# Kernel optimization log

Hardware: AMD Instinct MI355X
Metric: run time of the kernel (lower is better)

## Reference

```python
import jax, jax.numpy as jnp
import numpy as np

N = 131072
D = 512        # input_dim
H = 512        # hidden_dim
E = 10         # num_experts
INIT_STD_SCALE = 0.1


def _trunc_normal(key, shape, std):
    # approximate trunc_normal_(std=std) in [-2std, 2std]
    return jnp.clip(jax.random.normal(key, shape) * std, -2.0 * std, 2.0 * std).astype(jnp.float32)


def setup_inputs() -> dict:
    key = jax.random.key(0)
    ks = jax.random.split(key, 6)
    x = jax.random.normal(ks[0], (N, D), dtype=jnp.float32)
    # router (default nn.Linear init approximated with uniform)
    lim = 1.0 / np.sqrt(D)
    Wr = jax.random.uniform(ks[1], (E, D), minval=-lim, maxval=lim, dtype=jnp.float32)
    br = jnp.zeros((E,), dtype=jnp.float32)
    # experts: trunc_normal with std = 0.1 / sqrt(fan_in), zero bias
    W1 = _trunc_normal(ks[2], (E, D, H), INIT_STD_SCALE / np.sqrt(D))   # [E, D, H]
    b1 = jnp.zeros((E, H), dtype=jnp.float32)
    W2 = _trunc_normal(ks[3], (E, H, H), INIT_STD_SCALE / np.sqrt(H))   # [E, H, H]
    b2 = jnp.zeros((E, H), dtype=jnp.float32)
    return {"x": x, "Wr": Wr, "br": br, "W1": W1, "b1": b1, "W2": W2, "b2": b2}


def reference(x, Wr, br, W1, b1, W2, b2):
    # router in fp32 (autocast disabled in original)
    logits = x.astype(jnp.float32) @ Wr.T + br          # [N, E]
    expert_ids = jnp.argmax(logits, axis=1)              # [N]
    out = jnp.zeros((x.shape[0], W2.shape[-1]), dtype=x.dtype)
    # fixed small loop over experts; dropout is identity at inference
    for e in range(W1.shape[0]):
        h = jax.nn.relu(x @ W1[e] + b1[e])                # [N, H]
        o = h @ W2[e] + b2[e]                             # [N, H]
        out = jnp.where((expert_ids == e)[:, None], o, out)
    return out, expert_ids
```

## Files before the change

### kernel.cpp

```cpp
#include <hip/hip_runtime.h>
#include <hip/hip_bf16.h>

#define N_TOK 131072
#define DIM   512
#define HID   512
#define NEXP  10

using bf16x8 = __attribute__((ext_vector_type(8))) short;
using f32x4  = __attribute__((ext_vector_type(4))) float;

__device__ __forceinline__ short f2bf(float f) {
    union { float f; unsigned u; } v; v.f = f;
    unsigned u = v.u;
    return (short)((u + 0x7FFFu + ((u >> 16) & 1u)) >> 16);
}

#define GLOAD16(g, l) __builtin_amdgcn_global_load_lds( \
    (const __attribute__((address_space(1))) void*)(g),  \
    (__attribute__((address_space(3))) void*)(l), 16, 0, 0)

__global__ __launch_bounds__(256) void router_kernel(
    const float* __restrict__ x, const float* __restrict__ Wr,
    const float* __restrict__ br, int* __restrict__ eid,
    float* __restrict__ ids_out, int* __restrict__ counts)
{
    __shared__ float wr[NEXP][DIM];
    __shared__ int lcnt[NEXP];
    int tid = threadIdx.x;
    for (int i = tid; i < NEXP * DIM / 4; i += 256)
        ((float4*)wr)[i] = ((const float4*)Wr)[i];
    if (tid < NEXP) lcnt[tid] = 0;
    __syncthreads();

    int lane  = tid & 63;
    int wave  = tid >> 6;
    int gwave = blockIdx.x * 4 + wave;
    int nwav  = gridDim.x * 4;

    for (int t = gwave; t < N_TOK; t += nwav) {
        const float4* xr = (const float4*)(x + (size_t)t * DIM);
        float4 v0 = xr[lane * 2], v1 = xr[lane * 2 + 1];
        float xf[8] = {v0.x, v0.y, v0.z, v0.w, v1.x, v1.y, v1.z, v1.w};
        float dot[NEXP];
        #pragma unroll
        for (int e = 0; e < NEXP; ++e) {
            const float* wv = &wr[e][lane * 8];
            float s = 0.f;
            #pragma unroll
            for (int j = 0; j < 8; ++j) s = fmaf(xf[j], wv[j], s);
            dot[e] = s;
        }
        #pragma unroll
        for (int off = 32; off > 0; off >>= 1) {
            #pragma unroll
            for (int e = 0; e < NEXP; ++e) dot[e] += __shfl_xor(dot[e], off, 64);
        }
        if (lane == 0) {
            int best = 0; float bv = dot[0] + br[0];
            #pragma unroll
            for (int e = 1; e < NEXP; ++e) {
                float v = dot[e] + br[e];
                if (v > bv) { bv = v; best = e; }
            }
            eid[t] = best;
            ids_out[t] = (float)best;
            atomicAdd(&lcnt[best], 1);
        }
    }
    __syncthreads();
    if (tid < NEXP) atomicAdd(&counts[tid], lcnt[tid]);
}

__global__ void offsets_kernel(const int* __restrict__ counts,
                               int* __restrict__ offsets, int* __restrict__ toff)
{
    if (threadIdx.x == 0) {
        int acc = 0, ta = 0;
        for (int e = 0; e < NEXP; ++e) {
            offsets[e] = acc; toff[e] = ta;
            acc += counts[e]; ta += (counts[e] + 127) >> 7;
        }
        offsets[NEXP] = acc; toff[NEXP] = ta;
    }
}

__global__ __launch_bounds__(256) void scatter_kernel(
    const int* __restrict__ eid, const int* __restrict__ offsets,
    int* __restrict__ cursors, int* __restrict__ perm)
{
    __shared__ int lcnt[NEXP], lbase[NEXP];
    int tid = threadIdx.x;
    if (tid < NEXP) lcnt[tid] = 0;
    __syncthreads();
    int t = blockIdx.x * 256 + tid;
    int e = 0, lpos = 0;
    if (t < N_TOK) {
        e = eid[t];
        lpos = atomicAdd(&lcnt[e], 1);
    }
    __syncthreads();
    if (tid < NEXP) lbase[tid] = atomicAdd(&cursors[tid], lcnt[tid]);
    __syncthreads();
    if (t < N_TOK) perm[offsets[e] + lbase[e] + lpos] = t;
}

__global__ __launch_bounds__(256) void wconvert_kernel(
    const float* __restrict__ W1, const float* __restrict__ W2,
    short* __restrict__ W1bT, short* __restrict__ W2bT)
{
    int mat = blockIdx.z;
    const float* src = (mat < NEXP) ? W1 + (size_t)mat * 512 * 512
                                    : W2 + (size_t)(mat - NEXP) * 512 * 512;
    short* dst = (mat < NEXP) ? W1bT + (size_t)mat * 512 * 512
                              : W2bT + (size_t)(mat - NEXP) * 512 * 512;
    __shared__ float tile[64][65];
    int r0 = blockIdx.y * 64, c0 = blockIdx.x * 64;
    int tid = threadIdx.x;
    int tr = tid >> 4, tc4 = (tid & 15) * 4;
    #pragma unroll
    for (int i = 0; i < 4; ++i) {
        float4 v = *(const float4*)(src + (size_t)(r0 + i * 16 + tr) * 512 + c0 + tc4);
        tile[i * 16 + tr][tc4 + 0] = v.x; tile[i * 16 + tr][tc4 + 1] = v.y;
        tile[i * 16 + tr][tc4 + 2] = v.z; tile[i * 16 + tr][tc4 + 3] = v.w;
    }
    __syncthreads();
    #pragma unroll
    for (int i = 0; i < 4; ++i) {
        int cc = i * 16 + tr;
        ushort4 o;
        o.x = (ushort)f2bf(tile[tc4 + 0][cc]); o.y = (ushort)f2bf(tile[tc4 + 1][cc]);
        o.z = (ushort)f2bf(tile[tc4 + 2][cc]); o.w = (ushort)f2bf(tile[tc4 + 3][cc]);
        *(ushort4*)(dst + (size_t)(c0 + cc) * 512 + r0 + tc4) = o;
    }
}

template<int LAYER>
__global__ __launch_bounds__(512, 4) void expert_gemm(
    const float* __restrict__ x, const short* __restrict__ hA,
    const short* __restrict__ WT, const float* __restrict__ bias,
    const int* __restrict__ offsets, const int* __restrict__ toff,
    const int* __restrict__ perm,
    short* __restrict__ hOut, float* __restrict__ out)
{
    int g = blockIdx.x;
    if (g >= toff[NEXP]) return;
    int e = 0;
    #pragma unroll
    for (int k = 1; k < NEXP; ++k) e += (g >= toff[k]);
    int beg = offsets[e], cnt = offsets[e + 1] - beg;
    int m0 = (g - toff[e]) * 128;
    int nb = blockIdx.y * 256;

    __shared__ int toks[128];
    __shared__ short Abuf[2][128 * 32];
    __shared__ short Bbuf[2][256 * 32];

    int tid = threadIdx.x, lane = tid & 63, w = tid >> 6;
    if (tid < 128) toks[tid] = perm[beg + min(m0 + tid, cnt - 1)];
    __syncthreads();

    int arow = tid >> 2;
    int kq   = tid & 3;
    const float* xr   = nullptr;
    const short* ha   = nullptr;
    if (LAYER == 1) xr = x + (size_t)toks[arow] * DIM + kq * 8;
    else            ha = hA + (size_t)(beg + min(m0 + arow, cnt - 1)) * HID + kq * 8;
    const short* bp = WT + (size_t)e * 512 * 512 + (size_t)(nb + (tid >> 2)) * 512 + kq * 8;

    auto stage = [&](int t, int b) {
        char* bl = (char*)&Bbuf[b][0] + w * 1024;
        GLOAD16(bp + t * 32,         bl);
        GLOAD16(bp + t * 32 + 65536, bl + 8192);
        if (LAYER == 1) {
            float4 a0 = *(const float4*)(xr + t * 32);
            float4 a1 = *(const float4*)(xr + t * 32 + 4);
            bf16x8 p;
            p[0] = f2bf(a0.x); p[1] = f2bf(a0.y); p[2] = f2bf(a0.z); p[3] = f2bf(a0.w);
            p[4] = f2bf(a1.x); p[5] = f2bf(a1.y); p[6] = f2bf(a1.z); p[7] = f2bf(a1.w);
            *(bf16x8*)((char*)&Abuf[b][0] + tid * 16) = p;
        } else {
            GLOAD16(ha + t * 32, (char*)&Abuf[b][0] + w * 1024);
        }
    };

    f32x4 acc[4][4];
    #pragma unroll
    for (int i = 0; i < 4; ++i)
        #pragma unroll
        for (int j = 0; j < 4; ++j) acc[i][j] = (f32x4){0.f, 0.f, 0.f, 0.f};

    int wr = w >> 2, wc = w & 3;
    int lrow = lane & 15;
    int lk   = (lane >> 4) * 8;

    auto compute = [&](int b) {
        const short* A = &Abuf[b][0];
        const short* B = &Bbuf[b][0];
        bf16x8 af[4], bfv[4];
        #pragma unroll
        for (int i = 0; i < 4; ++i)
            af[i] = *(const bf16x8*)(A + (wr * 64 + i * 16 + lrow) * 32 + lk);
        #pragma unroll
        for (int j = 0; j < 4; ++j)
            bfv[j] = *(const bf16x8*)(B + (wc * 64 + j * 16 + lrow) * 32 + lk);
        #pragma unroll
        for (int i = 0; i < 4; ++i)
            #pragma unroll
            for (int j = 0; j < 4; ++j)
                acc[i][j] = __builtin_amdgcn_mfma_f32_16x16x32_bf16(af[i], bfv[j], acc[i][j], 0, 0, 0);
    };

    stage(0, 0);
    __syncthreads();
    #pragma unroll 1
    for (int t = 0; t < 14; t += 2) {
        stage(t + 1, 1); compute(0); __syncthreads();
        stage(t + 2, 0); compute(1); __syncthreads();
    }
    stage(15, 1); compute(0); __syncthreads();
    compute(1);

    const float* be = bias + (size_t)e * 512;
    int colb = nb + wc * 64 + lrow;
    float bv[4];
    #pragma unroll
    for (int j = 0; j < 4; ++j) bv[j] = be[colb + j * 16];

    #pragma unroll
    for (int i = 0; i < 4; ++i) {
        #pragma unroll
        for (int q = 0; q < 4; ++q) {
            int rr = wr * 64 + i * 16 + ((lane >> 4) << 2) + q;
            if (m0 + rr < cnt) {
                if (LAYER == 1) {
                    short* hp = hOut + (size_t)(beg + m0 + rr) * HID + colb;
                    #pragma unroll
                    for (int j = 0; j < 4; ++j) {
                        float v = acc[i][j][q] + bv[j];
                        hp[j * 16] = f2bf(v > 0.f ? v : 0.f);
                    }
                } else {
                    float* op = out + (size_t)toks[rr] * HID + colb;
                    #pragma unroll
                    for (int j = 0; j < 4; ++j)
                        op[j * 16] = acc[i][j][q] + bv[j];
                }
            }
        }
    }
}

extern "C" void kernel_launch(void* const* d_in, const int* in_sizes, int n_in,
                              void* d_out, int out_size, void* d_ws, size_t ws_size,
                              hipStream_t stream)
{
    const float* x  = (const float*)d_in[0];
    const float* Wr = (const float*)d_in[1];
    const float* br = (const float*)d_in[2];
    const float* W1 = (const float*)d_in[3];
    const float* b1 = (const float*)d_in[4];
    const float* W2 = (const float*)d_in[5];
    const float* b2 = (const float*)d_in[6];

    float* out     = (float*)d_out;
    float* ids_out = out + (size_t)N_TOK * HID;

    char* ws     = (char*)d_ws;
    int* counts  = (int*)ws;
    int* offsets = counts + 16;
    int* toff    = counts + 32;
    int* cursors = counts + 48;
    int* eid     = (int*)(ws + 1024);
    int* perm    = eid + N_TOK;
    short* W1bT  = (short*)(ws + 1024 + (size_t)2 * N_TOK * 4);
    short* W2bT  = W1bT + (size_t)NEXP * 512 * 512;
    short* h     = W2bT + (size_t)NEXP * 512 * 512;

    hipMemsetAsync(d_ws, 0, 1024, stream);
    router_kernel<<<2048, 256, 0, stream>>>(x, Wr, br, eid, ids_out, counts);
    wconvert_kernel<<<dim3(8, 8, 2 * NEXP), 256, 0, stream>>>(W1, W2, W1bT, W2bT);
    offsets_kernel<<<1, 64, 0, stream>>>(counts, offsets, toff);
    scatter_kernel<<<512, 256, 0, stream>>>(eid, offsets, cursors, perm);

    int ntiles = (N_TOK + 127) / 128 + NEXP;
    expert_gemm<1><<<dim3(ntiles, 2), 512, 0, stream>>>(x, nullptr, W1bT, b1, offsets, toff, perm, h, nullptr);
    expert_gemm<2><<<dim3(ntiles, 2), 512, 0, stream>>>(nullptr, h, W2bT, b2, offsets, toff, perm, nullptr, out);
}
```

Measured before the change: 434.4 us.

## Triple-buffer expert GEMM K-loop with XOR-swizzled LDS and explicit waitcnt barriers

Moves the expert GEMM mainloop from double to triple buffering. Loads run two K-steps ahead, with hand-placed s_waitcnt vmcnt and raw s_barrier so global loads stay in flight across compute. The LDS tiles get an XOR swizzle on the 16-byte k-chunk index to cut bank conflicts on the MFMA fragment reads, and the MFMA block is wrapped in s_setprio. The gain is more memory/compute overlap, at the cost of more LDS per block, which may lower occupancy. The hand-written waitcnt counts are fragile if the compiler reorders or merges loads.

```diff
diff --git a/kernel.cpp b/kernel.cpp
--- a/kernel.cpp
+++ b/kernel.cpp
@@ -14,6 +14,8 @@
     unsigned u = v.u;
     return (short)((u + 0x7FFFu + ((u >> 16) & 1u)) >> 16);
 }
+
+#define SWZ(r) (((r) ^ ((r) >> 2)) & 3)
 
 #define GLOAD16(g, l) __builtin_amdgcn_global_load_lds( \
     (const __attribute__((address_space(1))) void*)(g),  \
@@ -152,36 +154,57 @@
     int nb = blockIdx.y * 256;
 
     __shared__ int toks[128];
-    __shared__ short Abuf[2][128 * 32];
-    __shared__ short Bbuf[2][256 * 32];
+    __shared__ short Ab[3][128 * 32];
+    __shared__ short Bb[3][256 * 32];
 
     int tid = threadIdx.x, lane = tid & 63, w = tid >> 6;
     if (tid < 128) toks[tid] = perm[beg + min(m0 + tid, cnt - 1)];
     __syncthreads();
 
-    int arow = tid >> 2;
-    int kq   = tid & 3;
-    const float* xr   = nullptr;
-    const short* ha   = nullptr;
-    if (LAYER == 1) xr = x + (size_t)toks[arow] * DIM + kq * 8;
-    else            ha = hA + (size_t)(beg + min(m0 + arow, cnt - 1)) * HID + kq * 8;
-    const short* bp = WT + (size_t)e * 512 * 512 + (size_t)(nb + (tid >> 2)) * 512 + kq * 8;
-
-    auto stage = [&](int t, int b) {
-        char* bl = (char*)&Bbuf[b][0] + w * 1024;
-        GLOAD16(bp + t * 32,         bl);
-        GLOAD16(bp + t * 32 + 65536, bl + 8192);
-        if (LAYER == 1) {
-            float4 a0 = *(const float4*)(xr + t * 32);
-            float4 a1 = *(const float4*)(xr + t * 32 + 4);
-            bf16x8 p;
-            p[0] = f2bf(a0.x); p[1] = f2bf(a0.y); p[2] = f2bf(a0.z); p[3] = f2bf(a0.w);
-            p[4] = f2bf(a1.x); p[5] = f2bf(a1.y); p[6] = f2bf(a1.z); p[7] = f2bf(a1.w);
-            *(bf16x8*)((char*)&Abuf[b][0] + tid * 16) = p;
-        } else {
-            GLOAD16(ha + t * 32, (char*)&Abuf[b][0] + w * 1024);
-        }
-    };
+    const short* WTe = WT + (size_t)e * 512 * 512;
+    int srow  = w * 16 + (lane >> 2);
+    int kqp   = lane & 3;
+    int brow1 = 128 + srow;
+    const short* bSrc0 = WTe + (size_t)(nb + srow) * 512 + (kqp ^ SWZ(srow)) * 8;
+    const short* bSrc1 = WTe + (size_t)(nb + brow1) * 512 + (kqp ^ SWZ(brow1)) * 8;
+
+    const float* aSrcF = nullptr;
+    const short* aSrcH = nullptr;
+    int awrow = tid >> 2;
+    if (LAYER == 1)
+        aSrcF = x + (size_t)toks[awrow] * DIM + ((tid & 3) ^ SWZ(awrow)) * 8;
+    else
+        aSrcH = hA + (size_t)(beg + min(m0 + srow, cnt - 1)) * HID + (kqp ^ SWZ(srow)) * 8;
+
+    auto stageB = [&](int t, int b) {
+        GLOAD16(bSrc0 + t * 32, (char*)&Bb[b][0] + w * 1024);
+        GLOAD16(bSrc1 + t * 32, (char*)&Bb[b][0] + 8192 + w * 1024);
+    };
+    auto stageA2 = [&](int t, int b) {
+        GLOAD16(aSrcH + t * 32, (char*)&Ab[b][0] + w * 1024);
+    };
+
+    float4 aR[2][2];
+    auto loadA1 = [&](int t, int s) {
+        aR[s][0] = *(const float4*)(aSrcF + t * 32);
+        aR[s][1] = *(const float4*)(aSrcF + t * 32 + 4);
+    };
+    auto writeA1 = [&](int s, int b) {
+        bf16x8 p;
+        p[0] = f2bf(aR[s][0].x); p[1] = f2bf(aR[s][0].y);
+        p[2] = f2bf(aR[s][0].z); p[3] = f2bf(aR[s][0].w);
+        p[4] = f2bf(aR[s][1].x); p[5] = f2bf(aR[s][1].y);
+        p[6] = f2bf(aR[s][1].z); p[7] = f2bf(aR[s][1].w);
+        *(bf16x8*)(&Ab[b][tid * 8]) = p;
+    };
+
+    int wr = w >> 2, wc = w & 3;
+    int lrow = lane & 15, kqr = lane >> 4;
+    int offA[4], offB[4];
+    #pragma unroll
+    for (int i = 0; i < 4; ++i) { int mr = wr * 64 + i * 16 + lrow; offA[i] = mr * 32 + (kqr ^ SWZ(mr)) * 8; }
+    #pragma unroll
+    for (int j = 0; j < 4; ++j) { int nr = wc * 64 + j * 16 + lrow; offB[j] = nr * 32 + (kqr ^ SWZ(nr)) * 8; }
 
     f32x4 acc[4][4];
     #pragma unroll
@@ -189,36 +212,55 @@
         #pragma unroll
         for (int j = 0; j < 4; ++j) acc[i][j] = (f32x4){0.f, 0.f, 0.f, 0.f};
 
-    int wr = w >> 2, wc = w & 3;
-    int lrow = lane & 15;
-    int lk   = (lane >> 4) * 8;
-
-    auto compute = [&](int b) {
-        const short* A = &Abuf[b][0];
-        const short* B = &Bbuf[b][0];
-        bf16x8 af[4], bfv[4];
-        #pragma unroll
-        for (int i = 0; i < 4; ++i)
-            af[i] = *(const bf16x8*)(A + (wr * 64 + i * 16 + lrow) * 32 + lk);
-        #pragma unroll
-        for (int j = 0; j < 4; ++j)
-            bfv[j] = *(const bf16x8*)(B + (wc * 64 + j * 16 + lrow) * 32 + lk);
+    auto comp = [&](int b) {
+        bf16x8 af[4], bv[4];
+        #pragma unroll
+        for (int i = 0; i < 4; ++i) af[i] = *(const bf16x8*)&Ab[b][offA[i]];
+        #pragma unroll
+        for (int j = 0; j < 4; ++j) bv[j] = *(const bf16x8*)&Bb[b][offB[j]];
+        __builtin_amdgcn_s_setprio(1);
         #pragma unroll
         for (int i = 0; i < 4; ++i)
             #pragma unroll
             for (int j = 0; j < 4; ++j)
-                acc[i][j] = __builtin_amdgcn_mfma_f32_16x16x32_bf16(af[i], bfv[j], acc[i][j], 0, 0, 0);
-    };
-
-    stage(0, 0);
-    __syncthreads();
-    #pragma unroll 1
-    for (int t = 0; t < 14; t += 2) {
-        stage(t + 1, 1); compute(0); __syncthreads();
-        stage(t + 2, 0); compute(1); __syncthreads();
-    }
-    stage(15, 1); compute(0); __syncthreads();
-    compute(1);
+                acc[i][j] = __builtin_amdgcn_mfma_f32_16x16x32_bf16(af[i], bv[j], acc[i][j], 0, 0, 0);
+        __builtin_amdgcn_s_setprio(0);
+    };
+
+    if (LAYER == 1) {
+        loadA1(0, 0); stageB(0, 0); loadA1(1, 1); stageB(1, 1);
+        asm volatile("s_waitcnt vmcnt(4)" ::: "memory");
+        writeA1(0, 0);
+        asm volatile("s_waitcnt lgkmcnt(0)" ::: "memory");
+        __builtin_amdgcn_sched_barrier(0);
+    } else {
+        stageA2(0, 0); stageB(0, 0); stageA2(1, 1); stageB(1, 1);
+        asm volatile("s_waitcnt vmcnt(3)" ::: "memory");
+    }
+    __builtin_amdgcn_s_barrier();
+
+    #pragma unroll
+    for (int t = 0; t < 16; ++t) {
+        int cur = t % 3, wb = (t + 1) % 3, nx = (t + 2) % 3;
+        if (t + 2 < 16) {
+            if (LAYER == 1) loadA1(t + 2, t & 1);
+            else            stageA2(t + 2, nx);
+            stageB(t + 2, nx);
+        }
+        comp(cur);
+        if (t == 15) break;
+        if (LAYER == 1) {
+            if (t + 2 < 16) asm volatile("s_waitcnt vmcnt(4)" ::: "memory");
+            else            asm volatile("s_waitcnt vmcnt(0)" ::: "memory");
+            writeA1((t + 1) & 1, wb);
+            asm volatile("s_waitcnt lgkmcnt(0)" ::: "memory");
+            __builtin_amdgcn_sched_barrier(0);
+        } else {
+            if (t + 2 < 16) asm volatile("s_waitcnt vmcnt(3)" ::: "memory");
+            else            asm volatile("s_waitcnt vmcnt(0)" ::: "memory");
+        }
+        __builtin_amdgcn_s_barrier();
+    }
 
     const float* be = bias + (size_t)e * 512;
     int colb = nb + wc * 64 + lrow;
```

Result: slower. 521.8 us (+20.1%).

## Pre-convert x to bf16 in router, k-slab weight layout, triple-buffered GEMM pipeline

Applied to the files above, without the earlier changes.

The router kernel now also writes a bf16 copy of x, so the first expert GEMM loads A tiles straight into LDS with global_load_lds instead of converting fp32 in registers. Weights are stored in k-slab-major layout so each 32-wide K slice of B is contiguous. The GEMM main loop becomes a fully unrolled three-stage LDS pipeline that uses explicit vmcnt waits and raw barriers, and it raises wave priority around the MFMA blocks. The cost is an extra 128 MB bf16 write in the router plus more LDS per block, which may reduce occupancy.

```diff
diff --git a/kernel.cpp b/kernel.cpp
--- a/kernel.cpp
+++ b/kernel.cpp
@@ -22,7 +22,8 @@
 __global__ __launch_bounds__(256) void router_kernel(
     const float* __restrict__ x, const float* __restrict__ Wr,
     const float* __restrict__ br, int* __restrict__ eid,
-    float* __restrict__ ids_out, int* __restrict__ counts)
+    float* __restrict__ ids_out, int* __restrict__ counts,
+    short* __restrict__ xb)
 {
     __shared__ float wr[NEXP][DIM];
     __shared__ int lcnt[NEXP];
@@ -41,6 +42,11 @@
         const float4* xr = (const float4*)(x + (size_t)t * DIM);
         float4 v0 = xr[lane * 2], v1 = xr[lane * 2 + 1];
         float xf[8] = {v0.x, v0.y, v0.z, v0.w, v1.x, v1.y, v1.z, v1.w};
+        bf16x8 p;
+        #pragma unroll
+        for (int j = 0; j < 8; ++j) p[j] = f2bf(xf[j]);
+        *(bf16x8*)(xb + (size_t)t * DIM + lane * 8) = p;
+
         float dot[NEXP];
         #pragma unroll
         for (int e = 0; e < NEXP; ++e) {
@@ -106,13 +112,13 @@
 
 __global__ __launch_bounds__(256) void wconvert_kernel(
     const float* __restrict__ W1, const float* __restrict__ W2,
-    short* __restrict__ W1bT, short* __restrict__ W2bT)
+    short* __restrict__ W1b, short* __restrict__ W2b)
 {
     int mat = blockIdx.z;
     const float* src = (mat < NEXP) ? W1 + (size_t)mat * 512 * 512
                                     : W2 + (size_t)(mat - NEXP) * 512 * 512;
-    short* dst = (mat < NEXP) ? W1bT + (size_t)mat * 512 * 512
-                              : W2bT + (size_t)(mat - NEXP) * 512 * 512;
+    short* dst = (mat < NEXP) ? W1b + (size_t)mat * 512 * 512
+                              : W2b + (size_t)(mat - NEXP) * 512 * 512;
     __shared__ float tile[64][65];
     int r0 = blockIdx.y * 64, c0 = blockIdx.x * 64;
     int tid = threadIdx.x;
@@ -124,19 +130,21 @@
         tile[i * 16 + tr][tc4 + 2] = v.z; tile[i * 16 + tr][tc4 + 3] = v.w;
     }
     __syncthreads();
+    int s   = (r0 + tc4) >> 5;
+    int kin = (r0 + tc4) & 31;
     #pragma unroll
     for (int i = 0; i < 4; ++i) {
         int cc = i * 16 + tr;
         ushort4 o;
         o.x = (ushort)f2bf(tile[tc4 + 0][cc]); o.y = (ushort)f2bf(tile[tc4 + 1][cc]);
         o.z = (ushort)f2bf(tile[tc4 + 2][cc]); o.w = (ushort)f2bf(tile[tc4 + 3][cc]);
-        *(ushort4*)(dst + (size_t)(c0 + cc) * 512 + r0 + tc4) = o;
+        *(ushort4*)(dst + (size_t)s * 16384 + (size_t)(c0 + cc) * 32 + kin) = o;
     }
 }
 
 template<int LAYER>
 __global__ __launch_bounds__(512, 4) void expert_gemm(
-    const float* __restrict__ x, const short* __restrict__ hA,
+    const short* __restrict__ xb, const short* __restrict__ hA,
     const short* __restrict__ WT, const float* __restrict__ bias,
     const int* __restrict__ offsets, const int* __restrict__ toff,
     const int* __restrict__ perm,
@@ -152,35 +160,25 @@
     int nb = blockIdx.y * 256;
 
     __shared__ int toks[128];
-    __shared__ short Abuf[2][128 * 32];
-    __shared__ short Bbuf[2][256 * 32];
+    __shared__ short Ab[3][128 * 32];
+    __shared__ short Bb[3][256 * 32];
 
     int tid = threadIdx.x, lane = tid & 63, w = tid >> 6;
     if (tid < 128) toks[tid] = perm[beg + min(m0 + tid, cnt - 1)];
     __syncthreads();
 
-    int arow = tid >> 2;
-    int kq   = tid & 3;
-    const float* xr   = nullptr;
-    const short* ha   = nullptr;
-    if (LAYER == 1) xr = x + (size_t)toks[arow] * DIM + kq * 8;
-    else            ha = hA + (size_t)(beg + min(m0 + arow, cnt - 1)) * HID + kq * 8;
-    const short* bp = WT + (size_t)e * 512 * 512 + (size_t)(nb + (tid >> 2)) * 512 + kq * 8;
+    int srow = w * 16 + (lane >> 2);
+    int slot = lane & 3;
+    const short* WTe  = WT + (size_t)e * 512 * 512;
+    const short* bSrc = WTe + (size_t)(nb + srow) * 32 + slot * 8;
+    const short* aSrc;
+    if (LAYER == 1) aSrc = xb + (size_t)toks[srow] * DIM + slot * 8;
+    else            aSrc = hA + (size_t)(beg + min(m0 + srow, cnt - 1)) * HID + slot * 8;
 
     auto stage = [&](int t, int b) {
-        char* bl = (char*)&Bbuf[b][0] + w * 1024;
-        GLOAD16(bp + t * 32,         bl);
-        GLOAD16(bp + t * 32 + 65536, bl + 8192);
-        if (LAYER == 1) {
-            float4 a0 = *(const float4*)(xr + t * 32);
-            float4 a1 = *(const float4*)(xr + t * 32 + 4);
-            bf16x8 p;
-            p[0] = f2bf(a0.x); p[1] = f2bf(a0.y); p[2] = f2bf(a0.z); p[3] = f2bf(a0.w);
-            p[4] = f2bf(a1.x); p[5] = f2bf(a1.y); p[6] = f2bf(a1.z); p[7] = f2bf(a1.w);
-            *(bf16x8*)((char*)&Abuf[b][0] + tid * 16) = p;
-        } else {
-            GLOAD16(ha + t * 32, (char*)&Abuf[b][0] + w * 1024);
-        }
+        GLOAD16(bSrc + t * 16384,        (char*)&Bb[b][0] + w * 1024);
+        GLOAD16(bSrc + t * 16384 + 4096, (char*)&Bb[b][0] + 8192 + w * 1024);
+        GLOAD16(aSrc + t * 32,           (char*)&Ab[b][0] + w * 1024);
     };
 
     f32x4 acc[4][4];
@@ -193,32 +191,39 @@
     int lrow = lane & 15;
     int lk   = (lane >> 4) * 8;
 
-    auto compute = [&](int b) {
-        const short* A = &Abuf[b][0];
-        const short* B = &Bbuf[b][0];
-        bf16x8 af[4], bfv[4];
+    auto comp = [&](int b) {
+        const short* A = &Ab[b][0];
+        const short* B = &Bb[b][0];
+        bf16x8 af[4], bv[4];
         #pragma unroll
         for (int i = 0; i < 4; ++i)
             af[i] = *(const bf16x8*)(A + (wr * 64 + i * 16 + lrow) * 32 + lk);
         #pragma unroll
         for (int j = 0; j < 4; ++j)
-            bfv[j] = *(const bf16x8*)(B + (wc * 64 + j * 16 + lrow) * 32 + lk);
+            bv[j] = *(const bf16x8*)(B + (wc * 64 + j * 16 + lrow) * 32 + lk);
+        __builtin_amdgcn_s_setprio(1);
         #pragma unroll
         for (int i = 0; i < 4; ++i)
             #pragma unroll
             for (int j = 0; j < 4; ++j)
-                acc[i][j] = __builtin_amdgcn_mfma_f32_16x16x32_bf16(af[i], bfv[j], acc[i][j], 0, 0, 0);
+                acc[i][j] = __builtin_amdgcn_mfma_f32_16x16x32_bf16(af[i], bv[j], acc[i][j], 0, 0, 0);
+        __builtin_amdgcn_s_setprio(0);
     };
 
     stage(0, 0);
-    __syncthreads();
-    #pragma unroll 1
-    for (int t = 0; t < 14; t += 2) {
-        stage(t + 1, 1); compute(0); __syncthreads();
-        stage(t + 2, 0); compute(1); __syncthreads();
-    }
-    stage(15, 1); compute(0); __syncthreads();
-    compute(1);
+    stage(1, 1);
+    asm volatile("s_waitcnt vmcnt(3)" ::: "memory");
+    __builtin_amdgcn_s_barrier();
+
+    #pragma unroll
+    for (int t = 0; t < 16; ++t) {
+        if (t + 2 < 16) stage(t + 2, (t + 2) % 3);
+        comp(t % 3);
+        if (t == 15) break;
+        if (t + 2 < 16) asm volatile("s_waitcnt vmcnt(3)" ::: "memory");
+        else            asm volatile("s_waitcnt vmcnt(0)" ::: "memory");
+        __builtin_amdgcn_s_barrier();
+    }
 
     const float* be = bias + (size_t)e * 512;
     int colb = nb + wc * 64 + lrow;
@@ -272,17 +277,18 @@
     int* cursors = counts + 48;
     int* eid     = (int*)(ws + 1024);
     int* perm    = eid + N_TOK;
-    short* W1bT  = (short*)(ws + 1024 + (size_t)2 * N_TOK * 4);
-    short* W2bT  = W1bT + (size_t)NEXP * 512 * 512;
-    short* h     = W2bT + (size_t)NEXP * 512 * 512;
+    short* W1b   = (short*)(ws + 1024 + (size_t)2 * N_TOK * 4);
+    short* W2b   = W1b + (size_t)NEXP * 512 * 512;
+    short* h     = W2b + (size_t)NEXP * 512 * 512;
+    short* xb    = h   + (size_t)N_TOK * HID;
 
     hipMemsetAsync(d_ws, 0, 1024, stream);
-    router_kernel<<<2048, 256, 0, stream>>>(x, Wr, br, eid, ids_out, counts);
-    wconvert_kernel<<<dim3(8, 8, 2 * NEXP), 256, 0, stream>>>(W1, W2, W1bT, W2bT);
+    router_kernel<<<2048, 256, 0, stream>>>(x, Wr, br, eid, ids_out, counts, xb);
+    wconvert_kernel<<<dim3(8, 8, 2 * NEXP), 256, 0, stream>>>(W1, W2, W1b, W2b);
     offsets_kernel<<<1, 64, 0, stream>>>(counts, offsets, toff);
     scatter_kernel<<<512, 256, 0, stream>>>(eid, offsets, cursors, perm);
 
     int ntiles = (N_TOK + 127) / 128 + NEXP;
-    expert_gemm<1><<<dim3(ntiles, 2), 512, 0, stream>>>(x, nullptr, W1bT, b1, offsets, toff, perm, h, nullptr);
-    expert_gemm<2><<<dim3(ntiles, 2), 512, 0, stream>>>(nullptr, h, W2bT, b2, offsets, toff, perm, nullptr, out);
-}
+    expert_gemm<1><<<dim3(ntiles, 2), 512, 0, stream>>>(xb, nullptr, W1b, b1, offsets, toff, perm, h, nullptr);
+    expert_gemm<2><<<dim3(ntiles, 2), 512, 0, stream>>>(nullptr, h, W2b, b2, offsets, toff, perm, nullptr, out);
+}
```

After: 367.0 us. 15.5% less time.
